# Optimization experiments

Measured on AMD Instinct MI355X. Metric: run time of the kernel, lower is better.

## Reference

```python
import jax, jax.numpy as jnp
from jax import lax
import numpy as np

# pywt Wavelet('db4') decomposition filters
DEC_LO = jnp.array([-0.010597401784997278, 0.032883011666982945, 0.030841381835986965,
                    -0.18703481171888114, -0.027983769416983848, 0.6308807679295904,
                    0.7148465705525415, 0.23037781330885523], dtype=jnp.float32)
DEC_HI = jnp.array([-0.23037781330885523, 0.7148465705525415, -0.6308807679295904,
                    -0.027983769416983848, 0.18703481171888114, 0.030841381835986965,
                    -0.032883011666982945, -0.010597401784997278], dtype=jnp.float32)
FLT = 8
BN_INV = np.float32(1.0 / np.sqrt(1.0 + 1e-5))  # BatchNorm eval: running_mean=0, running_var=1


def dwt_db4(v):
    """Vectorized pywt.dwt(v, 'db4', mode='symmetric') along the last axis.
    v: (..., n) -> (cA, cD), each (..., (n+FLT-1)//2).
    pywt: symmetric-pad by FLT-1, true convolution with filter, take valid[1::2].
    Equivalent: correlate padded[1:...] with flipped filter, stride 2."""
    n = v.shape[-1]
    out_len = (n + FLT - 1) // 2
    xp = jnp.pad(v, [(0, 0)] * (v.ndim - 1) + [(FLT - 1, FLT - 1)], mode='symmetric')
    xp = xp[..., 1:1 + 2 * (out_len - 1) + FLT]
    lead = v.shape[:-1]
    xr = xp.reshape(-1, 1, xp.shape[-1])                      # (N*, 1, L)
    kern = jnp.stack([DEC_LO[::-1], DEC_HI[::-1]])[:, None, :]  # (2, 1, 8)
    y = lax.conv_general_dilated(xr, kern, (2,), 'VALID',
                                 dimension_numbers=('NCH', 'OIH', 'NCH'))
    return y[:, 0].reshape(lead + (out_len,)), y[:, 1].reshape(lead + (out_len,))


def conv_bn_relu(x, w, g, b):
    # x: (B, C, S); w: (O, I, K) no bias; BN in eval mode; ReLU; dropout off (eval)
    k = w.shape[-1]
    p = (k - 1) // 2
    y = lax.conv_general_dilated(x, w, (1,), [(p, p)],
                                 dimension_numbers=('NCH', 'OIH', 'NCH'))
    return jax.nn.relu((g * BN_INV)[None, :, None] * y + b[None, :, None])


def setup_inputs() -> dict:
    key = jax.random.key(0)
    ks = jax.random.split(key, 16)
    C, S, B = 88, 2048, 4
    d = dict()
    d['x'] = jax.random.normal(ks[0], (B, S, C), dtype=jnp.float32)
    d['w1'] = jax.random.normal(ks[1], (C, C, 1), dtype=jnp.float32) * 0.05
    d['w2a'] = jax.random.normal(ks[2], (C, C, 1), dtype=jnp.float32) * 0.05
    d['w2b'] = jax.random.normal(ks[3], (C, C, 3), dtype=jnp.float32) * 0.05
    d['w3a'] = jax.random.normal(ks[4], (C, C, 1), dtype=jnp.float32) * 0.05
    d['w3b'] = jax.random.normal(ks[5], (C, C, 3), dtype=jnp.float32) * 0.05
    d['w3c'] = jax.random.normal(ks[6], (C, C, 5), dtype=jnp.float32) * 0.05
    for nm in ['g1', 'g2a', 'g2b', 'g3a', 'g3b', 'g3c']:
        d[nm] = jnp.ones((C,), dtype=jnp.float32)
    for nm in ['b1', 'b2a', 'b2b', 'b3a', 'b3b', 'b3c']:
        d[nm] = jnp.zeros((C,), dtype=jnp.float32)
    d['Wmp'] = jax.random.normal(ks[7], (C, 3 * C), dtype=jnp.float32) * 0.05
    d['bmp'] = jnp.zeros((C,), dtype=jnp.float32)
    d['Wq'] = jax.random.normal(ks[8], (C, C), dtype=jnp.float32) * 0.1
    d['Wk'] = jax.random.normal(ks[9], (C, C), dtype=jnp.float32) * 0.1
    d['Wv'] = jax.random.normal(ks[10], (C, C), dtype=jnp.float32) * 0.1
    d['Wout'] = jax.random.normal(ks[11], (C, 112), dtype=jnp.float32) * 0.05
    d['bout'] = jnp.zeros((C,), dtype=jnp.float32)
    return d


def reference(x, w1, g1, b1, w2a, g2a, b2a, w2b, g2b, b2b,
              w3a, g3a, b3a, w3b, g3b, b3b, w3c, g3c, b3c,
              Wmp, bmp, Wq, Wk, Wv, Wout, bout):
    B, S, H = x.shape
    head = 4
    dk = H // head                                # 22
    wd = dk // 2 + 3 if dk % 2 == 0 else (dk + 1) // 2 + 3  # 14
    xt = jnp.swapaxes(x, 1, 2)                    # (B, C, S)
    # mutil_Parallel: three conv lines + fuse + residual
    x1 = conv_bn_relu(xt, w1, g1, b1)
    x2 = conv_bn_relu(conv_bn_relu(xt, w2a, g2a, b2a), w2b, g2b, b2b)
    x3 = conv_bn_relu(conv_bn_relu(conv_bn_relu(xt, w3a, g3a, b3a), w3b, g3b, b3b), w3c, g3c, b3c)
    cat = jnp.concatenate([x1, x2, x3], axis=1)   # (B, 3C, S)
    mp = jnp.einsum('bcs,oc->bso', cat, Wmp) + bmp + x  # (B, S, C)
    identity = mp
    # multi-head attention with wavelet-transformed values
    scale = dk ** (-0.5)
    q = jnp.einsum('bsh,oh->bso', mp, Wq).reshape(B, S, head, dk).transpose(0, 2, 1, 3) * scale
    k = jnp.einsum('bsh,oh->bso', mp, Wk).reshape(B, S, head, dk).transpose(0, 2, 1, 3)
    v = jnp.einsum('bsh,oh->bso', mp, Wv).reshape(B, S, head, dk).transpose(0, 2, 1, 3)
    attn = jax.nn.softmax(jnp.einsum('bhqd,bhkd->bhqk', q, k), axis=-1)  # (B,4,S,S)
    cA, cD = dwt_db4(v)                           # each (B, 4, S, 14)
    wcd = jnp.einsum('bhqk,bhkd->bhqd', attn, cD)  # (B, 4, S, 14)
    xo = jax.nn.relu(wcd.transpose(0, 2, 1, 3).reshape(B, S, head * wd))
    cAr = cA.reshape(B, S, head * wd)             # faithful to source's direct .view
    out = jnp.concatenate([xo, cAr], axis=-1) @ Wout.T + bout
    return identity + out
```

## Files before the change

### kernel.cpp

```cpp
#include <hip/hip_runtime.h>

#define BN_INV  0.99999500003749981f
#define QSCALE  0.21320071635561041f

typedef unsigned int uint;
typedef unsigned short u16;
typedef __attribute__((ext_vector_type(8))) short s16x8;
typedef __attribute__((ext_vector_type(4))) float f32x4;

#define OFF_BCAT 0
#define OFF_V    512
#define OFF_MP   721408
#define SW0    2884608
#define SB1    (SW0)
#define SB2B   (SW0+30720)
#define SB3B   (SW0+67584)
#define SB3C   (SW0+104448)
#define SBMP   (SW0+165888)
#define SBQKV  (SW0+202752)
#define SBOUT  (SW0+239616)
#define SXB    3148800
#define SXCAT  3869696
#define SX2    6032384
#define ST3B   6753280
#define SX3    7474176
#define SMPB   8195072
#define SQB    3869696
#define SKB    4918272
#define SCDT   5966848
#define SXOB   6753280

__constant__ float c_dlo[8] = {-0.010597401784997278f, 0.032883011666982945f,
    0.030841381835986965f, -0.18703481171888114f, -0.02798376941698385f,
    0.6308807679295904f, 0.7148465705525415f, 0.23037781330885523f};
__constant__ float c_dhi[8] = {-0.23037781330885523f, 0.7148465705525415f,
    -0.6308807679295904f, -0.02798376941698385f, 0.18703481171888114f,
    0.030841381835986965f, -0.032883011666982945f, -0.010597401784997278f};

__device__ __forceinline__ u16 f2bf(float f) {
    uint u = __float_as_uint(f);
    uint r = u + 0x7fffu + ((u >> 16) & 1u);
    return (u16)(r >> 16);
}

__global__ __launch_bounds__(256) void prepk(
    const float* __restrict__ x,
    const float* __restrict__ w1, const float* __restrict__ w2a, const float* __restrict__ w2b,
    const float* __restrict__ w3a, const float* __restrict__ w3b, const float* __restrict__ w3c,
    const float* __restrict__ g1, const float* __restrict__ g2a, const float* __restrict__ g2b,
    const float* __restrict__ g3a, const float* __restrict__ g3b, const float* __restrict__ g3c,
    const float* __restrict__ b1, const float* __restrict__ b2a, const float* __restrict__ b3a,
    const float* __restrict__ Wmp, const float* __restrict__ Wq, const float* __restrict__ Wk,
    const float* __restrict__ Wv, const float* __restrict__ Wout, float* __restrict__ ws)
{
    u16* wu = (u16*)ws;
    int r = blockIdx.x * 256 + threadIdx.x;
    if (r < 264) {
        ws[OFF_BCAT + r] = (r < 88) ? b1[r] : (r < 176 ? b2a[r-88] : b3a[r-176]);
        return;
    }
    r -= 264;
    if (r < 320*96) {
        int n = r / 96, kk = r % 96; float v = 0.f;
        if (kk < 88 && n < 264) {
            if (n < 88)       v = w1 [n*88+kk]       * g1 [n];
            else if (n < 176) v = w2a[(n-88)*88+kk]  * g2a[n-88];
            else              v = w3a[(n-176)*88+kk] * g3a[n-176];
            v *= BN_INV;
        }
        wu[SB1 + r] = f2bf(v); return;
    }
    r -= 320*96;
    if (r < 128*288) {
        int n = r / 288, kk = r % 288, t = kk/96, i = kk%96; float v = 0.f;
        if (n < 88 && i < 88) v = w2b[n*264 + i*3 + t] * g2b[n] * BN_INV;
        wu[SB2B + r] = f2bf(v); return;
    }
    r -= 128*288;
    if (r < 128*288) {
        int n = r / 288, kk = r % 288, t = kk/96, i = kk%96; float v = 0.f;
        if (n < 88 && i < 88) v = w3b[n*264 + i*3 + t] * g3b[n] * BN_INV;
        wu[SB3B + r] = f2bf(v); return;
    }
    r -= 128*288;
    if (r < 128*480) {
        int n = r / 480, kk = r % 480, t = kk/96, i = kk%96; float v = 0.f;
        if (n < 88 && i < 88) v = w3c[n*440 + i*5 + t] * g3c[n] * BN_INV;
        wu[SB3C + r] = f2bf(v); return;
    }
    r -= 128*480;
    if (r < 128*288) {
        int n = r / 288, kk = r % 288, c = kk/96, i = kk%96; float v = 0.f;
        if (n < 88 && i < 88) v = Wmp[n*264 + c*88 + i];
        wu[SBMP + r] = f2bf(v); return;
    }
    r -= 128*288;
    if (r < 384*96) {
        int n = r / 96, kk = r % 96, sec = n / 128, o = n % 128; float v = 0.f;
        if (o < 88 && kk < 88) {
            if (sec == 0)      v = Wq[o*88+kk] * QSCALE;
            else if (sec == 1) v = Wk[o*88+kk];
            else               v = Wv[o*88+kk];
        }
        wu[SBQKV + r] = f2bf(v); return;
    }
    r -= 384*96;
    if (r < 128*192) {
        int n = r / 192, kk = r % 192; float v = 0.f;
        if (n < 88 && kk < 112) v = Wout[n*112 + kk];
        wu[SBOUT + r] = f2bf(v); return;
    }
    r -= 128*192;
    if (r < 8192*88) {
        wu[SXB + r] = f2bf(x[r]); return;
    }
}

struct GemmChunks {
    int soff[5];
    int stride[5];
    int shift[5];
    int cols[5];
};

template<int NCH, int MODE, int OUTM>
__global__ __launch_bounds__(256) void gemmk(GemmChunks ch,
    const u16* __restrict__ wsrc,
    const u16* __restrict__ Bw, const u16* __restrict__ Bw2, int Ktot,
    const float* __restrict__ bias, const float* __restrict__ bias2,
    const float* __restrict__ resid, int relu,
    u16* __restrict__ outb, u16* __restrict__ outb2,
    float* __restrict__ outf, int outStride, int N)
{
    __shared__ u16 As[64*104];
    __shared__ u16 Bs[64*104];
    int tid = threadIdx.x;
    int lane = tid & 63, w = tid >> 6, wr = w >> 1, wc = w & 1;
    int p0 = blockIdx.x * 64;
    int nb = blockIdx.y;
    int which = (MODE == 2) ? (nb >> 1) : 0;
    int nbl   = (MODE == 2) ? (nb & 1) : nb;
    const u16* Bw_ = (MODE == 2 && which) ? Bw2 : Bw;
    int bs = p0 & ~2047, be = bs + 2048;

    f32x4 acc[2][2];
    #pragma unroll
    for (int a = 0; a < 2; a++)
        #pragma unroll
        for (int b = 0; b < 2; b++) acc[a][b] = (f32x4){0.f,0.f,0.f,0.f};

    int ar0 = (wr*32 + (lane&15))*104 + (lane>>4)*8;
    int br0 = (wc*32 + (lane&15))*104 + (lane>>4)*8;

    for (int c = 0; c < NCH; c++) {
        int soff = ch.soff[c] + which*88;
        int stride = ch.stride[c], shift = ch.shift[c], cols = ch.cols[c];
        __syncthreads();
        for (int e = tid; e < 768; e += 256) {
            int r = e / 12, seg = e % 12;
            int row = p0 + r + shift;
            int4 val = {0,0,0,0};
            if (row >= bs && row < be && seg*8 < cols)
                val = *(const int4*)&wsrc[(size_t)soff + (size_t)row*stride + seg*8];
            *(int4*)&As[r*104 + seg*8] = val;
        }
        for (int e = tid; e < 768; e += 256) {
            int n = e / 12, seg = e % 12;
            *(int4*)&Bs[n*104 + seg*8] =
                *(const int4*)&Bw_[((size_t)(nbl*64 + n))*Ktot + c*96 + seg*8];
        }
        __syncthreads();
        #pragma unroll
        for (int ks = 0; ks < 3; ks++) {
            s16x8 a0 = *(const s16x8*)&As[ar0 + ks*32];
            s16x8 a1 = *(const s16x8*)&As[ar0 + 16*104 + ks*32];
            s16x8 b0 = *(const s16x8*)&Bs[br0 + ks*32];
            s16x8 b1 = *(const s16x8*)&Bs[br0 + 16*104 + ks*32];
            acc[0][0] = __builtin_amdgcn_mfma_f32_16x16x32_bf16(a0, b0, acc[0][0], 0, 0, 0);
            acc[0][1] = __builtin_amdgcn_mfma_f32_16x16x32_bf16(a0, b1, acc[0][1], 0, 0, 0);
            acc[1][0] = __builtin_amdgcn_mfma_f32_16x16x32_bf16(a1, b0, acc[1][0], 0, 0, 0);
            acc[1][1] = __builtin_amdgcn_mfma_f32_16x16x32_bf16(a1, b1, acc[1][1], 0, 0, 0);
        }
    }

    int rbase = p0 + wr*32 + (lane>>4)*4;
    if (MODE != 1) {
        u16* outb_ = (MODE == 2 && which) ? outb2 : outb;
        const float* bias_ = (MODE == 2 && which) ? bias2 : bias;
        int cbase = nbl*64 + wc*32 + (lane&15);
        #pragma unroll
        for (int fn = 0; fn < 2; fn++) {
            int col = cbase + fn*16;
            if (col < N) {
                float bb = bias_ ? bias_[col] : 0.f;
                #pragma unroll
                for (int fm = 0; fm < 2; fm++)
                    #pragma unroll
                    for (int j = 0; j < 4; j++) {
                        int row = rbase + fm*16 + j;
                        float v = acc[fm][fn][j] + bb;
                        if (relu) v = fmaxf(v, 0.f);
                        if (resid) v += resid[(size_t)row*outStride + col];
                        if (OUTM & 1) outb_[(size_t)row*outStride + col] = f2bf(v);
                        if (OUTM & 2) outf[(size_t)row*outStride + col] = v;
                    }
            }
        }
    } else {
        u16* wq = outb;
        int sec = nb >> 1;
        #pragma unroll
        for (int fn = 0; fn < 2; fn++) {
            int cw = (nb&1)*64 + wc*32 + fn*16 + (lane&15);
            if (cw < 88) {
                int h = cw / 22, d = cw % 22;
                #pragma unroll
                for (int fm = 0; fm < 2; fm++)
                    #pragma unroll
                    for (int j = 0; j < 4; j++) {
                        int row = rbase + fm*16 + j;
                        int b = row >> 11, s = row & 2047;
                        float v = acc[fm][fn][j];
                        if (sec == 0)
                            wq[SQB + ((size_t)(b*4+h)*2048 + s)*32 + d] = f2bf(v);
                        else if (sec == 1)
                            wq[SKB + ((size_t)(b*4+h)*2048 + s)*32 + d] = f2bf(v);
                        else
                            outf[OFF_V + (size_t)row*88 + cw] = v;
                    }
            }
        }
    }
}

__global__ __launch_bounds__(256) void dwtk(float* __restrict__ ws)
{
    u16* wu = (u16*)ws;
    int tid = threadIdx.x;
    int p0 = blockIdx.x * 16;
    const float* V = ws + OFF_V;
    for (int e = tid; e < 896; e += 256) {
        int p = e / 56, rr = e % 56, h = rr / 14, jj = rr % 14;
        int pos = p0 + p, b = pos >> 11, s = pos & 2047;
        const float* v = &V[(size_t)pos*88 + h*22];
        float ca = 0.f, cd = 0.f;
        #pragma unroll
        for (int t = 0; t < 8; t++) {
            int pp = 1 + 2*jj + t;
            int oi = pp < 7 ? 6 - pp : (pp < 29 ? pp - 7 : 50 - pp);
            float vv = v[oi];
            ca = fmaf(vv, c_dlo[7-t], ca);
            cd = fmaf(vv, c_dhi[7-t], cd);
        }
        wu[SCDT + ((size_t)((b*4+h)*16 + jj))*2048 + s] = f2bf(cd);
        int hs = h*2048 + s, s2 = hs >> 2, qd = hs & 3;
        wu[SXOB + ((size_t)b*2048 + s2)*112 + 56 + qd*14 + jj] = f2bf(ca);
    }
    uint* wi = (uint*)ws;
    for (int e = tid; e < 640; e += 256) {
        int p = e / 40, t = e % 40;
        int h = t / 10, rest = t % 10, arr = rest / 5, ui = rest % 5;
        int pos = p0 + p, b = pos >> 11, s = pos & 2047;
        size_t base = (size_t)((arr ? SKB : SQB) >> 1) + ((size_t)(b*4+h)*2048 + s)*16;
        wi[base + 11 + ui] = 0;
    }
    for (int e = tid; e < 128; e += 256) {
        int p = e / 8, t = e % 8, h = t >> 1, dd = 14 + (t & 1);
        int pos = p0 + p, b = pos >> 11, s = pos & 2047;
        wu[SCDT + ((size_t)((b*4+h)*16 + dd))*2048 + s] = 0;
    }
}

__global__ __launch_bounds__(256) void attnk(float* __restrict__ ws)
{
    const u16* wu = (const u16*)ws;
    u16* wua = (u16*)ws;
    __shared__ __align__(16) u16 Kt[128*40];
    __shared__ __align__(16) u16 CDt[16*136];
    __shared__ __align__(16) u16 Pb[4][16*136];
    __shared__ float cb[4][16];
    __shared__ float lb[4][16];
    int tid = threadIdx.x, lane = tid & 63, w = tid >> 6;
    int bh = blockIdx.y;
    int q0 = blockIdx.x * 64 + w * 16;
    int qrow = lane & 15, grp = lane >> 4;

    s16x8 qf = *(const s16x8*)&wu[SQB + ((size_t)bh*2048 + q0 + qrow)*32 + grp*8];
    const u16* Kbase = wu + SKB + (size_t)bh*2048*32;
    const u16* Cbase = wu + SCDT + (size_t)bh*16*2048;

    f32x4 o = (f32x4){0.f,0.f,0.f,0.f};
    float m = -1e30f, l = 0.f;

    for (int kt = 0; kt < 16; kt++) {
        __syncthreads();
        for (int e = tid; e < 512; e += 256) {
            int r = e >> 2, seg = e & 3;
            *(int4*)&Kt[r*40 + seg*8] = *(const int4*)&Kbase[(size_t)(kt*128 + r)*32 + seg*8];
        }
        {
            int d = tid >> 4, seg = tid & 15;
            *(int4*)&CDt[d*136 + seg*8] = *(const int4*)&Cbase[(size_t)d*2048 + kt*128 + seg*8];
        }
        __syncthreads();

        f32x4 s4[8];
        #pragma unroll
        for (int sub = 0; sub < 8; sub++) {
            s16x8 kf = *(const s16x8*)&Kt[(sub*16 + qrow)*40 + grp*8];
            s4[sub] = __builtin_amdgcn_mfma_f32_16x16x32_bf16(kf, qf,
                        (f32x4){0.f,0.f,0.f,0.f}, 0, 0, 0);
        }
        float sv[32];
        #pragma unroll
        for (int sub = 0; sub < 8; sub++)
            #pragma unroll
            for (int j = 0; j < 4; j++) sv[sub*4+j] = s4[sub][j];

        float mx[16];
        #pragma unroll
        for (int i = 0; i < 16; i++) mx[i] = fmaxf(sv[i], sv[i+16]);
        #pragma unroll
        for (int i = 0; i < 8; i++) mx[i] = fmaxf(mx[i], mx[i+8]);
        #pragma unroll
        for (int i = 0; i < 4; i++) mx[i] = fmaxf(mx[i], mx[i+4]);
        float tm = fmaxf(fmaxf(mx[0], mx[1]), fmaxf(mx[2], mx[3]));
        tm = fmaxf(tm, __shfl_xor(tm, 16));
        tm = fmaxf(tm, __shfl_xor(tm, 32));
        float mn = fmaxf(m, tm);
        float corr = __expf(m - mn);
        m = mn;

        float pv[32];
        #pragma unroll
        for (int i = 0; i < 32; i++) pv[i] = __expf(sv[i] - mn);
        float sm[16];
        #pragma unroll
        for (int i = 0; i < 16; i++) sm[i] = pv[i] + pv[i+16];
        #pragma unroll
        for (int i = 0; i < 8; i++) sm[i] += sm[i+8];
        #pragma unroll
        for (int i = 0; i < 4; i++) sm[i] += sm[i+4];
        float ls = (sm[0] + sm[1]) + (sm[2] + sm[3]);
        ls += __shfl_xor(ls, 16);
        ls += __shfl_xor(ls, 32);
        l = l * corr + ls;

        if (lane < 16) cb[w][lane] = corr;
        __builtin_amdgcn_s_waitcnt(0);
        {
            const float* cp = &cb[w][grp*4];
            #pragma unroll
            for (int j = 0; j < 4; j++) o[j] *= cp[j];
        }
        {
            uint* pb32 = (uint*)Pb[w];
            #pragma unroll
            for (int sub = 0; sub < 8; sub++) {
                uint u01 = (uint)f2bf(pv[sub*4+0]) | ((uint)f2bf(pv[sub*4+1]) << 16);
                uint u23 = (uint)f2bf(pv[sub*4+2]) | ((uint)f2bf(pv[sub*4+3]) << 16);
                int sa = qrow*136 + sub*16 + grp*4;
                pb32[sa >> 1] = u01;
                pb32[(sa >> 1) + 1] = u23;
            }
        }
        #pragma unroll
        for (int ks = 0; ks < 4; ks++) {
            s16x8 pa = *(const s16x8*)&Pb[w][qrow*136 + ks*32 + grp*8];
            s16x8 cf = *(const s16x8*)&CDt[qrow*136 + ks*32 + grp*8];
            o = __builtin_amdgcn_mfma_f32_16x16x32_bf16(pa, cf, o, 0, 0, 0);
        }
    }

    if (lane < 16) lb[w][lane] = l;
    __builtin_amdgcn_s_waitcnt(0);
    {
        const float* lp = &lb[w][grp*4];
        int b = bh >> 2, h = bh & 3, d = qrow;
        if (d < 14) {
            #pragma unroll
            for (int j = 0; j < 4; j++) {
                int s = q0 + grp*4 + j;
                float val = o[j] / lp[j];
                wua[SXOB + ((size_t)b*2048 + s)*112 + h*14 + d] = f2bf(fmaxf(val, 0.f));
            }
        }
    }
}

extern "C" void kernel_launch(void* const* d_in, const int* in_sizes, int n_in,
                              void* d_out, int out_size, void* d_ws, size_t ws_size,
                              hipStream_t stream) {
    const float* x    = (const float*)d_in[0];
    const float* w1   = (const float*)d_in[1];
    const float* w2a  = (const float*)d_in[2];
    const float* w2b  = (const float*)d_in[3];
    const float* w3a  = (const float*)d_in[4];
    const float* w3b  = (const float*)d_in[5];
    const float* w3c  = (const float*)d_in[6];
    const float* g1   = (const float*)d_in[7];
    const float* g2a  = (const float*)d_in[8];
    const float* g2b  = (const float*)d_in[9];
    const float* g3a  = (const float*)d_in[10];
    const float* g3b  = (const float*)d_in[11];
    const float* g3c  = (const float*)d_in[12];
    const float* b1   = (const float*)d_in[13];
    const float* b2a  = (const float*)d_in[14];
    const float* b2b  = (const float*)d_in[15];
    const float* b3a  = (const float*)d_in[16];
    const float* b3b  = (const float*)d_in[17];
    const float* b3c  = (const float*)d_in[18];
    const float* Wmp  = (const float*)d_in[19];
    const float* bmp  = (const float*)d_in[20];
    const float* Wq   = (const float*)d_in[21];
    const float* Wk   = (const float*)d_in[22];
    const float* Wv   = (const float*)d_in[23];
    const float* Wout = (const float*)d_in[24];
    const float* bout = (const float*)d_in[25];
    float* ws = (float*)d_ws;
    float* out = (float*)d_out;
    u16* wu = (u16*)d_ws;

    prepk<<<3850, 256, 0, stream>>>(x, w1, w2a, w2b, w3a, w3b, w3c,
                                    g1, g2a, g2b, g3a, g3b, g3c,
                                    b1, b2a, b3a, Wmp, Wq, Wk, Wv, Wout, ws);

    {
        GemmChunks c{}; c.soff[0]=SXB; c.stride[0]=88; c.shift[0]=0; c.cols[0]=88;
        gemmk<1,0,1><<<dim3(128,5), 256, 0, stream>>>(c, wu, wu+SB1, nullptr, 96,
            ws+OFF_BCAT, nullptr, nullptr, 1, wu+SXCAT, nullptr, nullptr, 264, 264);
    }
    {
        GemmChunks c{};
        for (int t = 0; t < 3; t++) { c.soff[t]=SXCAT+88; c.stride[t]=264; c.shift[t]=t-1; c.cols[t]=88; }
        gemmk<3,2,1><<<dim3(128,4), 256, 0, stream>>>(c, wu, wu+SB2B, wu+SB3B, 288,
            b2b, b3b, nullptr, 1, wu+SX2, wu+ST3B, nullptr, 88, 88);
    }
    {
        GemmChunks c{};
        for (int t = 0; t < 5; t++) { c.soff[t]=ST3B; c.stride[t]=88; c.shift[t]=t-2; c.cols[t]=88; }
        gemmk<5,0,1><<<dim3(128,2), 256, 0, stream>>>(c, wu, wu+SB3C, nullptr, 480,
            b3c, nullptr, nullptr, 1, wu+SX3, nullptr, nullptr, 88, 88);
    }
    {
        GemmChunks c{};
        c.soff[0]=SXCAT; c.stride[0]=264; c.shift[0]=0; c.cols[0]=88;
        c.soff[1]=SX2;   c.stride[1]=88;  c.shift[1]=0; c.cols[1]=88;
        c.soff[2]=SX3;   c.stride[2]=88;  c.shift[2]=0; c.cols[2]=88;
        gemmk<3,0,3><<<dim3(128,2), 256, 0, stream>>>(c, wu, wu+SBMP, nullptr, 288,
            bmp, nullptr, x, 0, wu+SMPB, nullptr, ws+OFF_MP, 88, 88);
    }
    {
        GemmChunks c{}; c.soff[0]=SMPB; c.stride[0]=88; c.shift[0]=0; c.cols[0]=88;
        gemmk<1,1,0><<<dim3(128,6), 256, 0, stream>>>(c, wu, wu+SBQKV, nullptr, 96,
            nullptr, nullptr, nullptr, 0, wu, nullptr, ws, 0, 0);
    }
    dwtk<<<512, 256, 0, stream>>>(ws);
    attnk<<<dim3(32, 16), 256, 0, stream>>>(ws);
    {
        GemmChunks c{};
        c.soff[0]=SXOB;    c.stride[0]=112; c.shift[0]=0; c.cols[0]=96;
        c.soff[1]=SXOB+96; c.stride[1]=112; c.shift[1]=0; c.cols[1]=16;
        gemmk<2,0,2><<<dim3(128,2), 256, 0, stream>>>(c, wu, wu+SBOUT, nullptr, 192,
            bout, nullptr, ws+OFF_MP, 0, nullptr, nullptr, out, 88, 88);
    }
}
```

Measured before the change: 210.4 us.

## Split attention keys across two wave groups and prefetch GEMM chunks into registers

The attention kernel now runs 512 threads per block. Two groups of four waves each process half of the key range, with a split-softmax merge through shared memory at the end, and a lazy rescale that skips the correction when the running max barely changes. The GEMM kernel prefetches the next K-chunk's A/B tiles into registers while MFMAs run on the current chunk. This is meant to raise occupancy and latency hiding in attention and overlap global loads in the GEMMs, at the cost of extra barriers and register pressure.

```diff
diff --git a/kernel.cpp b/kernel.cpp
--- a/kernel.cpp
+++ b/kernel.cpp
@@ -152,24 +152,34 @@
     int ar0 = (wr*32 + (lane&15))*104 + (lane>>4)*8;
     int br0 = (wc*32 + (lane&15))*104 + (lane>>4)*8;
 
-    for (int c = 0; c < NCH; c++) {
+    int4 ra[3], rb[3];
+    auto loadC = [&](int c) {
         int soff = ch.soff[c] + which*88;
         int stride = ch.stride[c], shift = ch.shift[c], cols = ch.cols[c];
-        __syncthreads();
-        for (int e = tid; e < 768; e += 256) {
+        #pragma unroll
+        for (int t = 0; t < 3; t++) {
+            int e = tid + t*256;
             int r = e / 12, seg = e % 12;
             int row = p0 + r + shift;
-            int4 val = {0,0,0,0};
+            int4 v = {0,0,0,0};
             if (row >= bs && row < be && seg*8 < cols)
-                val = *(const int4*)&wsrc[(size_t)soff + (size_t)row*stride + seg*8];
-            *(int4*)&As[r*104 + seg*8] = val;
-        }
-        for (int e = tid; e < 768; e += 256) {
-            int n = e / 12, seg = e % 12;
-            *(int4*)&Bs[n*104 + seg*8] =
-                *(const int4*)&Bw_[((size_t)(nbl*64 + n))*Ktot + c*96 + seg*8];
+                v = *(const int4*)&wsrc[(size_t)soff + (size_t)row*stride + seg*8];
+            ra[t] = v;
+            rb[t] = *(const int4*)&Bw_[((size_t)(nbl*64 + r))*Ktot + c*96 + seg*8];
+        }
+    };
+
+    loadC(0);
+    for (int c = 0; c < NCH; c++) {
+        #pragma unroll
+        for (int t = 0; t < 3; t++) {
+            int e = tid + t*256;
+            int r = e / 12, seg = e % 12;
+            *(int4*)&As[r*104 + seg*8] = ra[t];
+            *(int4*)&Bs[r*104 + seg*8] = rb[t];
         }
         __syncthreads();
+        if (c + 1 < NCH) loadC(c + 1);
         #pragma unroll
         for (int ks = 0; ks < 3; ks++) {
             s16x8 a0 = *(const s16x8*)&As[ar0 + ks*32];
@@ -181,6 +191,7 @@
             acc[1][0] = __builtin_amdgcn_mfma_f32_16x16x32_bf16(a1, b0, acc[1][0], 0, 0, 0);
             acc[1][1] = __builtin_amdgcn_mfma_f32_16x16x32_bf16(a1, b1, acc[1][1], 0, 0, 0);
         }
+        __syncthreads();
     }
 
     int rbase = p0 + wr*32 + (lane>>4)*4;
@@ -271,117 +282,128 @@
     }
 }
 
-__global__ __launch_bounds__(256) void attnk(float* __restrict__ ws)
+__global__ __launch_bounds__(512, 4) void attnk(float* __restrict__ ws)
 {
     const u16* wu = (const u16*)ws;
     u16* wua = (u16*)ws;
-    __shared__ __align__(16) u16 Kt[128*40];
-    __shared__ __align__(16) u16 CDt[16*136];
-    __shared__ __align__(16) u16 Pb[4][16*136];
-    __shared__ float cb[4][16];
-    __shared__ float lb[4][16];
+    __shared__ __align__(16) u16 Kt[2*64*40];
+    __shared__ __align__(16) u16 CDt[2*16*72];
+    __shared__ __align__(16) u16 Pb[8][16*72];
+    __shared__ float cb[8][16];
     int tid = threadIdx.x, lane = tid & 63, w = tid >> 6;
     int bh = blockIdx.y;
-    int q0 = blockIdx.x * 64 + w * 16;
+    int qsub = w & 3, half = w >> 2;
+    int q0 = blockIdx.x * 64 + qsub * 16;
     int qrow = lane & 15, grp = lane >> 4;
 
     s16x8 qf = *(const s16x8*)&wu[SQB + ((size_t)bh*2048 + q0 + qrow)*32 + grp*8];
     const u16* Kbase = wu + SKB + (size_t)bh*2048*32;
     const u16* Cbase = wu + SCDT + (size_t)bh*16*2048;
+    const u16* Kh = &Kt[half*2560];
+    const u16* Ch = &CDt[half*1152];
 
     f32x4 o = (f32x4){0.f,0.f,0.f,0.f};
     float m = -1e30f, l = 0.f;
 
     for (int kt = 0; kt < 16; kt++) {
         __syncthreads();
-        for (int e = tid; e < 512; e += 256) {
-            int r = e >> 2, seg = e & 3;
-            *(int4*)&Kt[r*40 + seg*8] = *(const int4*)&Kbase[(size_t)(kt*128 + r)*32 + seg*8];
-        }
         {
-            int d = tid >> 4, seg = tid & 15;
-            *(int4*)&CDt[d*136 + seg*8] = *(const int4*)&Cbase[(size_t)d*2048 + kt*128 + seg*8];
+            int hh = tid >> 8, rr = (tid >> 2) & 63, seg = tid & 3;
+            *(int4*)&Kt[hh*2560 + rr*40 + seg*8] =
+                *(const int4*)&Kbase[(size_t)(hh*1024 + kt*64 + rr)*32 + seg*8];
+        }
+        if (tid < 256) {
+            int hh = tid >> 7, d = (tid >> 3) & 15, seg = tid & 7;
+            *(int4*)&CDt[hh*1152 + d*72 + seg*8] =
+                *(const int4*)&Cbase[(size_t)d*2048 + hh*1024 + kt*64 + seg*8];
         }
         __syncthreads();
 
-        f32x4 s4[8];
-        #pragma unroll
-        for (int sub = 0; sub < 8; sub++) {
-            s16x8 kf = *(const s16x8*)&Kt[(sub*16 + qrow)*40 + grp*8];
+        f32x4 s4[4];
+        #pragma unroll
+        for (int sub = 0; sub < 4; sub++) {
+            s16x8 kf = *(const s16x8*)&Kh[(sub*16 + qrow)*40 + grp*8];
             s4[sub] = __builtin_amdgcn_mfma_f32_16x16x32_bf16(kf, qf,
                         (f32x4){0.f,0.f,0.f,0.f}, 0, 0, 0);
         }
-        float sv[32];
-        #pragma unroll
-        for (int sub = 0; sub < 8; sub++)
+        float sv[16];
+        #pragma unroll
+        for (int sub = 0; sub < 4; sub++)
             #pragma unroll
             for (int j = 0; j < 4; j++) sv[sub*4+j] = s4[sub][j];
 
-        float mx[16];
-        #pragma unroll
-        for (int i = 0; i < 16; i++) mx[i] = fmaxf(sv[i], sv[i+16]);
-        #pragma unroll
-        for (int i = 0; i < 8; i++) mx[i] = fmaxf(mx[i], mx[i+8]);
+        float mx[8];
+        #pragma unroll
+        for (int i = 0; i < 8; i++) mx[i] = fmaxf(sv[i], sv[i+8]);
         #pragma unroll
         for (int i = 0; i < 4; i++) mx[i] = fmaxf(mx[i], mx[i+4]);
         float tm = fmaxf(fmaxf(mx[0], mx[1]), fmaxf(mx[2], mx[3]));
         tm = fmaxf(tm, __shfl_xor(tm, 16));
         tm = fmaxf(tm, __shfl_xor(tm, 32));
-        float mn = fmaxf(m, tm);
-        float corr = __expf(m - mn);
-        m = mn;
-
-        float pv[32];
-        #pragma unroll
-        for (int i = 0; i < 32; i++) pv[i] = __expf(sv[i] - mn);
-        float sm[16];
-        #pragma unroll
-        for (int i = 0; i < 16; i++) sm[i] = pv[i] + pv[i+16];
-        #pragma unroll
-        for (int i = 0; i < 8; i++) sm[i] += sm[i+8];
+
+        if (!__all(tm <= m + 8.f)) {
+            float mn = fmaxf(m, tm);
+            float corr = __expf(m - mn);
+            m = mn; l *= corr;
+            if (lane < 16) cb[w][lane] = corr;
+            __builtin_amdgcn_s_waitcnt(0);
+            const float* cp = &cb[w][grp*4];
+            #pragma unroll
+            for (int j = 0; j < 4; j++) o[j] *= cp[j];
+        }
+
+        float pv[16];
+        #pragma unroll
+        for (int i = 0; i < 16; i++) pv[i] = __expf(sv[i] - m);
+        float sm[8];
+        #pragma unroll
+        for (int i = 0; i < 8; i++) sm[i] = pv[i] + pv[i+8];
         #pragma unroll
         for (int i = 0; i < 4; i++) sm[i] += sm[i+4];
         float ls = (sm[0] + sm[1]) + (sm[2] + sm[3]);
         ls += __shfl_xor(ls, 16);
         ls += __shfl_xor(ls, 32);
-        l = l * corr + ls;
-
-        if (lane < 16) cb[w][lane] = corr;
-        __builtin_amdgcn_s_waitcnt(0);
-        {
-            const float* cp = &cb[w][grp*4];
-            #pragma unroll
-            for (int j = 0; j < 4; j++) o[j] *= cp[j];
-        }
+        l += ls;
+
         {
             uint* pb32 = (uint*)Pb[w];
             #pragma unroll
-            for (int sub = 0; sub < 8; sub++) {
+            for (int sub = 0; sub < 4; sub++) {
                 uint u01 = (uint)f2bf(pv[sub*4+0]) | ((uint)f2bf(pv[sub*4+1]) << 16);
                 uint u23 = (uint)f2bf(pv[sub*4+2]) | ((uint)f2bf(pv[sub*4+3]) << 16);
-                int sa = qrow*136 + sub*16 + grp*4;
-                pb32[sa >> 1] = u01;
-                pb32[(sa >> 1) + 1] = u23;
+                int sa = qrow*72 + sub*16 + grp*4;
+                *(uint2*)&pb32[sa >> 1] = make_uint2(u01, u23);
             }
         }
         #pragma unroll
-        for (int ks = 0; ks < 4; ks++) {
-            s16x8 pa = *(const s16x8*)&Pb[w][qrow*136 + ks*32 + grp*8];
-            s16x8 cf = *(const s16x8*)&CDt[qrow*136 + ks*32 + grp*8];
+        for (int ks = 0; ks < 2; ks++) {
+            s16x8 pa = *(const s16x8*)&Pb[w][qrow*72 + ks*32 + grp*8];
+            s16x8 cf = *(const s16x8*)&Ch[qrow*72 + ks*32 + grp*8];
             o = __builtin_amdgcn_mfma_f32_16x16x32_bf16(pa, cf, o, 0, 0, 0);
         }
     }
 
-    if (lane < 16) lb[w][lane] = l;
-    __builtin_amdgcn_s_waitcnt(0);
-    {
-        const float* lp = &lb[w][grp*4];
-        int b = bh >> 2, h = bh & 3, d = qrow;
-        if (d < 14) {
-            #pragma unroll
-            for (int j = 0; j < 4; j++) {
-                int s = q0 + grp*4 + j;
-                float val = o[j] / lp[j];
+    __syncthreads();
+    float* part = (float*)Kt;
+    if (lane < 16) { part[(w*16+lane)*18 + 0] = m; part[(w*16+lane)*18 + 1] = l; }
+    #pragma unroll
+    for (int j = 0; j < 4; j++) part[(w*16 + grp*4 + j)*18 + 2 + qrow] = o[j];
+    __syncthreads();
+    if (w < 4) {
+        int q = qrow;
+        const float* pa = &part[(w*16 + q)*18];
+        const float* pb = &part[((w+4)*16 + q)*18];
+        float m0 = pa[0], l0 = pa[1], m1 = pb[0], l1 = pb[1];
+        float M = fmaxf(m0, m1);
+        float e0 = __expf(m0 - M), e1 = __expf(m1 - M);
+        float inv = 1.f / (l0*e0 + l1*e1);
+        int b = bh >> 2, h = bh & 3;
+        int s = blockIdx.x * 64 + w * 16 + q;
+        #pragma unroll
+        for (int dd = 0; dd < 4; dd++) {
+            int d = grp*4 + dd;
+            if (d < 14) {
+                float val = (pa[2+d]*e0 + pb[2+d]*e1) * inv;
                 wua[SXOB + ((size_t)b*2048 + s)*112 + h*14 + d] = f2bf(fmaxf(val, 0.f));
             }
         }
@@ -456,7 +478,7 @@
             nullptr, nullptr, nullptr, 0, wu, nullptr, ws, 0, 0);
     }
     dwtk<<<512, 256, 0, stream>>>(ws);
-    attnk<<<dim3(32, 16), 256, 0, stream>>>(ws);
+    attnk<<<dim3(32, 16), 512, 0, stream>>>(ws);
     {
         GemmChunks c{};
         c.soff[0]=SXOB;    c.stride[0]=112; c.shift[0]=0; c.cols[0]=96;
```

After: 202.9 us. -3.6%, faster.
